# Performance work log

Hardware: AMD Instinct MI355X
Metric: run time of the kernel (lower is better)

## Reference

```python
import jax, jax.numpy as jnp
import numpy as np

EPS = 1e-12  # F.normalize default eps

def _l2norm(a, axis):
    n = jnp.sqrt(jnp.sum(a * a, axis=axis, keepdims=True))
    return a / jnp.maximum(n, EPS)

def setup_inputs() -> dict:
    key = jax.random.key(0)
    kx, kc = jax.random.split(key)
    x = jax.random.normal(kx, (32, 64, 64, 64), dtype=jnp.float32)        # [B,C,H,W]
    codebook = 0.2 * jax.random.normal(kc, (512, 64), dtype=jnp.float32)  # nn.init.normal_(w, 0, 0.2)
    return {"x": x, "codebook": codebook}

def reference(x, codebook):
    # mode == 'angular': normalize codebook rows and x along dim=1 (channels)
    cb = _l2norm(codebook, axis=1)          # [K,C]
    xn = _l2norm(x, axis=1)                 # [B,C,H,W]
    # x.transpose(-1, dim) with dim=1 -> swap axes 1 and 3
    xt = jnp.swapaxes(xn, 1, -1)            # [B,W,H,C]
    B, W, H, C = xt.shape
    flat = xt.reshape(-1, C)                # [N,C]
    d = (jnp.sum(cb * cb, axis=1)[None, :]
         + jnp.sum(flat * flat, axis=1, keepdims=True)
         - 2.0 * flat @ cb.T)               # [N,K]
    idx = jnp.argmin(d, axis=1)             # [N]
    codes = cb[idx].reshape(B, W, H, C)
    indices = idx.reshape(B, W, H)
    codes = jnp.swapaxes(codes, 1, -1)      # back to [B,C,H,W]
    indices = jnp.swapaxes(indices, 1, -1)  # [B,H,W]
    return codes, indices
```

## Files before the change

### kernel.cpp

```cpp
#include <hip/hip_runtime.h>

#define VQ_EPS    1e-12f
#define VQ_WINDOW 0.01f
#define VQ_CAP    12

typedef short bf16x8 __attribute__((ext_vector_type(8)));
typedef float f32x4  __attribute__((ext_vector_type(4)));

static __device__ __forceinline__ unsigned short f2bf(float f) {
    unsigned u = __float_as_uint(f);
    u += 0x7fffu + ((u >> 16) & 1u);
    return (unsigned short)(u >> 16);
}

static __device__ __forceinline__ unsigned f2ord(float f) {
    unsigned b = __float_as_uint(f);
    return (b & 0x80000000u) ? ~b : (b | 0x80000000u);
}

__global__ __launch_bounds__(64) void cb_prep_kernel(const float* __restrict__ cb,
                                                     float* __restrict__ cbn,
                                                     unsigned short* __restrict__ cbB,
                                                     float* __restrict__ kn2,
                                                     float* __restrict__ kn2p) {
    const int k = blockIdx.x;
    const int c = threadIdx.x;
    float v = cb[k * 64 + c];
    float s = v * v;
    #pragma unroll
    for (int off = 32; off > 0; off >>= 1) s += __shfl_xor(s, off, 64);
    float n = sqrtf(s);
    float cn = v / fmaxf(n, VQ_EPS);
    cbn[k * 64 + c] = cn;

    const int ntile = k >> 4, col = k & 15;
    const int ks = c >> 5, quad = (c >> 3) & 3, j = c & 7;
    cbB[(((ntile * 2 + ks) * 64) + quad * 16 + col) * 8 + j] = f2bf(cn);

    float s2 = cn * cn;
    #pragma unroll
    for (int off = 32; off > 0; off >>= 1) s2 += __shfl_xor(s2, off, 64);
    if (c == 0) { kn2[k] = s2; kn2p[k] = s2 + 2.0f; }
}

__global__ __launch_bounds__(256) void vq_mfma_kernel(const float* __restrict__ x,
                                                      const float* __restrict__ cbn,
                                                      const unsigned short* __restrict__ cbB,
                                                      const float* __restrict__ kn2,
                                                      const float* __restrict__ kn2p,
                                                      float* __restrict__ codes,
                                                      float* __restrict__ idxout) {
    __shared__ int    scnt[64];
    __shared__ int    slist[64][VQ_CAP];
    __shared__ unsigned long long spack[64];

    const int t    = threadIdx.x;
    const int lane = t & 63;
    const int wid  = t >> 6;
    const int col  = lane & 15;
    const int quad = lane >> 4;
    const int wpix = wid * 16 + col;

    const int rowid = blockIdx.x;
    const int b = rowid >> 6;
    const int h = rowid & 63;
    const float* xblk = x + ((size_t)b << 18) + (h << 6);

    if (quad == 0) { scnt[wpix] = 0; spack[wpix] = 0xFFFFFFFFFFFFFFFFull; }

    float xv[16];
    #pragma unroll
    for (int ks = 0; ks < 2; ++ks)
        #pragma unroll
        for (int j = 0; j < 8; ++j)
            xv[ks * 8 + j] = xblk[(size_t)(ks * 32 + quad * 8 + j) * 4096 + wpix];

    float ssp = 0.0f;
    #pragma unroll
    for (int i = 0; i < 16; ++i) ssp = fmaf(xv[i], xv[i], ssp);
    ssp += __shfl_xor(ssp, 16);
    ssp += __shfl_xor(ssp, 32);
    const float m2a = -2.0f * (1.0f / fmaxf(sqrtf(ssp), VQ_EPS));
    float m2r[4];
    #pragma unroll
    for (int r = 0; r < 4; ++r) m2r[r] = __shfl(m2a, quad * 4 + r);
    const float m2P = __shfl(m2a, lane >> 2);

    bf16x8 afrag[2];
    #pragma unroll
    for (int ks = 0; ks < 2; ++ks)
        #pragma unroll
        for (int j = 0; j < 8; ++j)
            ((unsigned short*)&afrag[ks])[j] = f2bf(xv[ks * 8 + j]);

    const bf16x8* gBf = (const bf16x8*)cbB;

    unsigned run1[4] = {0xFFFFFFFFu, 0xFFFFFFFFu, 0xFFFFFFFFu, 0xFFFFFFFFu};
    unsigned run2[4] = {0xFFFFFFFFu, 0xFFFFFFFFu, 0xFFFFFFFFu, 0xFFFFFFFFu};
    #pragma unroll 4
    for (int nt = 0; nt < 32; ++nt) {
        bf16x8 b0 = gBf[(nt * 2 + 0) * 64 + lane];
        bf16x8 b1 = gBf[(nt * 2 + 1) * 64 + lane];
        f32x4 c = {0.0f, 0.0f, 0.0f, 0.0f};
        c = __builtin_amdgcn_mfma_f32_16x16x32_bf16(afrag[0], b0, c, 0, 0, 0);
        c = __builtin_amdgcn_mfma_f32_16x16x32_bf16(afrag[1], b1, c, 0, 0, 0);
        const float    kn   = kn2p[nt * 16 + col];
        const unsigned kidx = (unsigned)(nt * 16 + col);
        #pragma unroll
        for (int r = 0; r < 4; ++r) {
            float s = fmaf(m2r[r], c[r], kn);
            unsigned key = (__float_as_uint(s) & 0xFFFFFE00u) | kidx;
            unsigned mx  = max(run1[r], key);
            run1[r] = min(run1[r], key);
            run2[r] = min(run2[r], mx);
        }
    }

    float thr[4];
    #pragma unroll
    for (int r = 0; r < 4; ++r) {
        unsigned v = run1[r];
        v = min(v, (unsigned)__shfl_xor((int)v, 1));
        v = min(v, (unsigned)__shfl_xor((int)v, 2));
        v = min(v, (unsigned)__shfl_xor((int)v, 4));
        v = min(v, (unsigned)__shfl_xor((int)v, 8));
        thr[r] = __uint_as_float(v & 0xFFFFFE00u) + VQ_WINDOW;
    }

    bool f = false;
    #pragma unroll
    for (int r = 0; r < 4; ++r)
        f |= (__uint_as_float(run2[r] & 0xFFFFFE00u) <= thr[r]);
    const unsigned long long waveflag = __ballot(f);

    if (waveflag != 0ull) {
        #pragma unroll 4
        for (int nt = 0; nt < 32; ++nt) {
            bf16x8 b0 = gBf[(nt * 2 + 0) * 64 + lane];
            bf16x8 b1 = gBf[(nt * 2 + 1) * 64 + lane];
            f32x4 c = {0.0f, 0.0f, 0.0f, 0.0f};
            c = __builtin_amdgcn_mfma_f32_16x16x32_bf16(afrag[0], b0, c, 0, 0, 0);
            c = __builtin_amdgcn_mfma_f32_16x16x32_bf16(afrag[1], b1, c, 0, 0, 0);
            const float kn   = kn2p[nt * 16 + col];
            const int   kidx = nt * 16 + col;
            #pragma unroll
            for (int r = 0; r < 4; ++r) {
                float s = fmaf(m2r[r], c[r], kn);
                if (s <= thr[r]) {
                    int pix = wid * 16 + quad * 4 + r;
                    int pos = atomicAdd(&scnt[pix], 1);
                    if (pos < VQ_CAP) slist[pix][pos] = kidx;
                }
            }
        }
    } else {
        #pragma unroll
        for (int r = 0; r < 4; ++r) {
            float s1 = __uint_as_float(run1[r] & 0xFFFFFE00u);
            if (s1 <= thr[r]) {
                int pix = wid * 16 + quad * 4 + r;
                int pos = atomicAdd(&scnt[pix], 1);
                if (pos < VQ_CAP) slist[pix][pos] = (int)(run1[r] & 0x1FFu);
            }
        }
    }
    __syncthreads();

    {
        const int P   = wid * 16 + (lane >> 2);
        const int sub = lane & 3;
        const int cnt = scnt[P];
        if (cnt > 1) {
            const float* xp = xblk + P;
            if (cnt <= VQ_CAP) {
                for (int i = sub; i < cnt; i += 4) {
                    const int k = slist[P][i];
                    const float* cr = cbn + (size_t)k * 64;
                    float dot = 0.0f;
                    #pragma unroll 8
                    for (int c = 0; c < 64; ++c)
                        dot = fmaf(xp[(size_t)c * 4096], cr[c], dot);
                    float s = fmaf(m2P, dot, kn2[k]);
                    unsigned long long key =
                        ((unsigned long long)f2ord(s) << 32) | (unsigned)k;
                    atomicMin(&spack[P], key);
                }
            } else {
                for (int k = sub; k < 512; k += 4) {
                    const float* cr = cbn + (size_t)k * 64;
                    float dot = 0.0f;
                    #pragma unroll 8
                    for (int c = 0; c < 64; ++c)
                        dot = fmaf(xp[(size_t)c * 4096], cr[c], dot);
                    float s = fmaf(m2P, dot, kn2[k]);
                    unsigned long long key =
                        ((unsigned long long)f2ord(s) << 32) | (unsigned)k;
                    atomicMin(&spack[P], key);
                }
            }
        }
    }
    __syncthreads();

    const int cntw = scnt[wpix];
    const int bk = (cntw == 1) ? slist[wpix][0]
                               : (int)(spack[wpix] & 0xFFFFFFFFull);

    if (quad == 0) idxout[rowid * 64 + wpix] = (float)bk;

    {
        const float4* crow = (const float4*)(cbn + (size_t)bk * 64) + quad * 4;
        float* cp = codes + ((size_t)b << 18) + (h << 6) + wpix;
        #pragma unroll
        for (int q = 0; q < 4; ++q) {
            float4 v = crow[q];
            const int c0 = quad * 16 + q * 4;
            cp[(size_t)(c0 + 0) * 4096] = v.x;
            cp[(size_t)(c0 + 1) * 4096] = v.y;
            cp[(size_t)(c0 + 2) * 4096] = v.z;
            cp[(size_t)(c0 + 3) * 4096] = v.w;
        }
    }
}

extern "C" void kernel_launch(void* const* d_in, const int* in_sizes, int n_in,
                              void* d_out, int out_size, void* d_ws, size_t ws_size,
                              hipStream_t stream) {
    const float* x  = (const float*)d_in[0];
    const float* cb = (const float*)d_in[1];

    float*          cbn  = (float*)d_ws;
    unsigned short* cbB  = (unsigned short*)(cbn + 512 * 64);
    float*          kn2  = (float*)(cbB + 32768);
    float*          kn2p = kn2 + 512;

    float* codes  = (float*)d_out;
    float* idxout = codes + (size_t)32 * 64 * 64 * 64;

    cb_prep_kernel<<<512, 64, 0, stream>>>(cb, cbn, cbB, kn2, kn2p);
    vq_mfma_kernel<<<2048, 256, 0, stream>>>(x, cbn, cbB, kn2, kn2p, codes, idxout);
}
```

Measured before the change: 130.0 us.

## Stage bf16 codebook in LDS and process two rows per block

Each block now copies the full 64 KB bf16 codebook fragment layout into shared memory once and reads the MFMA B-operands from LDS instead of global/L2. To amortize the copy, blocks grow to 512 threads and each handles two image rows, halving the grid. The cost is 64 KB+ of LDS per block, which limits occupancy to about two blocks per CU, plus an extra barrier before the main loop.

Measured after the change: 122.6 us. 1.06x faster.

```diff
diff --git a/kernel.cpp b/kernel.cpp
--- a/kernel.cpp
+++ b/kernel.cpp
@@ -43,30 +43,35 @@
     if (c == 0) { kn2[k] = s2; kn2p[k] = s2 + 2.0f; }
 }
 
-__global__ __launch_bounds__(256) void vq_mfma_kernel(const float* __restrict__ x,
+__global__ __launch_bounds__(512) void vq_mfma_kernel(const float* __restrict__ x,
                                                       const float* __restrict__ cbn,
                                                       const unsigned short* __restrict__ cbB,
                                                       const float* __restrict__ kn2,
                                                       const float* __restrict__ kn2p,
                                                       float* __restrict__ codes,
                                                       float* __restrict__ idxout) {
-    __shared__ int    scnt[64];
-    __shared__ int    slist[64][VQ_CAP];
-    __shared__ unsigned long long spack[64];
+    __shared__ __align__(16) unsigned short lcb[32768];
+    __shared__ unsigned long long spack[128];
+    __shared__ int slist[128][VQ_CAP];
+    __shared__ int scnt[128];
 
     const int t    = threadIdx.x;
     const int lane = t & 63;
     const int wid  = t >> 6;
     const int col  = lane & 15;
     const int quad = lane >> 4;
-    const int wpix = wid * 16 + col;
-
-    const int rowid = blockIdx.x;
+    const int wr   = wid & 3;
+    const int rsel = wid >> 2;
+    const int wpix = wr * 16 + col;
+    const int pbase = rsel * 64;
+    const int pslot = pbase + wpix;
+
+    const int rowid = blockIdx.x * 2 + rsel;
     const int b = rowid >> 6;
     const int h = rowid & 63;
     const float* xblk = x + ((size_t)b << 18) + (h << 6);
 
-    if (quad == 0) { scnt[wpix] = 0; spack[wpix] = 0xFFFFFFFFFFFFFFFFull; }
+    if (quad == 0) { scnt[pslot] = 0; spack[pslot] = 0xFFFFFFFFFFFFFFFFull; }
 
     float xv[16];
     #pragma unroll
@@ -74,6 +79,13 @@
         #pragma unroll
         for (int j = 0; j < 8; ++j)
             xv[ks * 8 + j] = xblk[(size_t)(ks * 32 + quad * 8 + j) * 4096 + wpix];
+
+    {
+        const uint4* g4 = (const uint4*)cbB;
+        uint4*       l4 = (uint4*)lcb;
+        #pragma unroll
+        for (int r = 0; r < 8; ++r) l4[r * 512 + t] = g4[r * 512 + t];
+    }
 
     float ssp = 0.0f;
     #pragma unroll
@@ -93,14 +105,16 @@
         for (int j = 0; j < 8; ++j)
             ((unsigned short*)&afrag[ks])[j] = f2bf(xv[ks * 8 + j]);
 
-    const bf16x8* gBf = (const bf16x8*)cbB;
+    __syncthreads();
+
+    const bf16x8* lBf = (const bf16x8*)lcb;
 
     unsigned run1[4] = {0xFFFFFFFFu, 0xFFFFFFFFu, 0xFFFFFFFFu, 0xFFFFFFFFu};
     unsigned run2[4] = {0xFFFFFFFFu, 0xFFFFFFFFu, 0xFFFFFFFFu, 0xFFFFFFFFu};
     #pragma unroll 4
     for (int nt = 0; nt < 32; ++nt) {
-        bf16x8 b0 = gBf[(nt * 2 + 0) * 64 + lane];
-        bf16x8 b1 = gBf[(nt * 2 + 1) * 64 + lane];
+        bf16x8 b0 = lBf[(nt * 2 + 0) * 64 + lane];
+        bf16x8 b1 = lBf[(nt * 2 + 1) * 64 + lane];
         f32x4 c = {0.0f, 0.0f, 0.0f, 0.0f};
         c = __builtin_amdgcn_mfma_f32_16x16x32_bf16(afrag[0], b0, c, 0, 0, 0);
         c = __builtin_amdgcn_mfma_f32_16x16x32_bf16(afrag[1], b1, c, 0, 0, 0);
@@ -136,8 +150,8 @@
     if (waveflag != 0ull) {
         #pragma unroll 4
         for (int nt = 0; nt < 32; ++nt) {
-            bf16x8 b0 = gBf[(nt * 2 + 0) * 64 + lane];
-            bf16x8 b1 = gBf[(nt * 2 + 1) * 64 + lane];
+            bf16x8 b0 = lBf[(nt * 2 + 0) * 64 + lane];
+            bf16x8 b1 = lBf[(nt * 2 + 1) * 64 + lane];
             f32x4 c = {0.0f, 0.0f, 0.0f, 0.0f};
             c = __builtin_amdgcn_mfma_f32_16x16x32_bf16(afrag[0], b0, c, 0, 0, 0);
             c = __builtin_amdgcn_mfma_f32_16x16x32_bf16(afrag[1], b1, c, 0, 0, 0);
@@ -147,7 +161,7 @@
             for (int r = 0; r < 4; ++r) {
                 float s = fmaf(m2r[r], c[r], kn);
                 if (s <= thr[r]) {
-                    int pix = wid * 16 + quad * 4 + r;
+                    int pix = pbase + wr * 16 + quad * 4 + r;
                     int pos = atomicAdd(&scnt[pix], 1);
                     if (pos < VQ_CAP) slist[pix][pos] = kidx;
                 }
@@ -158,7 +172,7 @@
         for (int r = 0; r < 4; ++r) {
             float s1 = __uint_as_float(run1[r] & 0xFFFFFE00u);
             if (s1 <= thr[r]) {
-                int pix = wid * 16 + quad * 4 + r;
+                int pix = pbase + wr * 16 + quad * 4 + r;
                 int pos = atomicAdd(&scnt[pix], 1);
                 if (pos < VQ_CAP) slist[pix][pos] = (int)(run1[r] & 0x1FFu);
             }
@@ -167,11 +181,12 @@
     __syncthreads();
 
     {
-        const int P   = wid * 16 + (lane >> 2);
-        const int sub = lane & 3;
-        const int cnt = scnt[P];
+        const int pw   = wr * 16 + (lane >> 2);
+        const int P    = pbase + pw;
+        const int sub  = lane & 3;
+        const int cnt  = scnt[P];
         if (cnt > 1) {
-            const float* xp = xblk + P;
+            const float* xp = xblk + pw;
             if (cnt <= VQ_CAP) {
                 for (int i = sub; i < cnt; i += 4) {
                     const int k = slist[P][i];
@@ -202,9 +217,9 @@
     }
     __syncthreads();
 
-    const int cntw = scnt[wpix];
-    const int bk = (cntw == 1) ? slist[wpix][0]
-                               : (int)(spack[wpix] & 0xFFFFFFFFull);
+    const int cntw = scnt[pslot];
+    const int bk = (cntw == 1) ? slist[pslot][0]
+                               : (int)(spack[pslot] & 0xFFFFFFFFull);
 
     if (quad == 0) idxout[rowid * 64 + wpix] = (float)bk;
 
@@ -238,5 +253,5 @@
     float* idxout = codes + (size_t)32 * 64 * 64 * 64;
 
     cb_prep_kernel<<<512, 64, 0, stream>>>(cb, cbn, cbB, kn2, kn2p);
-    vq_mfma_kernel<<<2048, 256, 0, stream>>>(x, cbn, cbB, kn2, kn2p, codes, idxout);
-}
+    vq_mfma_kernel<<<1024, 512, 0, stream>>>(x, cbn, cbB, kn2, kn2p, codes, idxout);
+}
```
